# Performance work log

Hardware: AMD Instinct MI355X
Metric: run time of the kernel (lower is better)

Reference implementation:

```python
import jax, jax.numpy as jnp
import numpy as np

N, K, C_S, C_Z, C_G, H, NUM_RBF = 768, 32, 384, 128, 16, 4, 64
E = N * K
DH = C_Z // H  # 32
LN_EPS = 1e-5
DIST_EPS = 1e-8


def _rbf(D, D_min=0.0, D_max=20.0, D_count=NUM_RBF):
    # Gaussian radial basis expansion (GVP/ProteinMPNN style)
    mu = jnp.linspace(D_min, D_max, D_count, dtype=D.dtype)
    sigma = (D_max - D_min) / D_count
    return jnp.exp(-(((D[..., None] - mu) / sigma) ** 2))


def setup_inputs() -> dict:
    key = jax.random.key(0)
    ks = jax.random.split(key, 24)
    node_features = jax.random.normal(ks[0], (N, C_S), dtype=jnp.float32)
    node_trans = jax.random.uniform(ks[1], (N, 3), dtype=jnp.float32) * 30.0  # coords in a 30A box
    edge_features = jax.random.normal(ks[2], (E, C_Z), dtype=jnp.float32)
    src = jax.random.randint(ks[3], (E,), 0, N)
    dst = jnp.repeat(jnp.arange(N), K)  # sorted-by-destination layout (assume_sorted)
    edge_index = jnp.stack([src, dst]).astype(jnp.int64)

    def lin(k, fan_in, fan_out, scale=0.02):
        return jax.random.normal(k, (fan_in, fan_out), dtype=jnp.float32) * scale

    return {
        "node_features": node_features,
        "node_trans": node_trans,
        "edge_features": edge_features,
        "edge_index": edge_index,
        "w_left": lin(ks[4], C_S, C_G), "b_left": jnp.zeros((C_G,), jnp.float32),
        "w_right": lin(ks[5], C_S, C_G), "b_right": jnp.zeros((C_G,), jnp.float32),
        "w_bgate": lin(ks[6], C_G * C_G, C_Z), "b_bgate": jnp.zeros((C_Z,), jnp.float32),
        "w_dist": lin(ks[7], NUM_RBF, C_Z), "b_dist": jnp.zeros((C_Z,), jnp.float32),
        "w_tobias": lin(ks[8], C_Z, H),
        "ln_g": jnp.ones((C_Z,), jnp.float32), "ln_b": jnp.zeros((C_Z,), jnp.float32),
        "w_q": lin(ks[9], C_Z, C_Z), "b_q": jnp.zeros((C_Z,), jnp.float32),
        "w_kv": lin(ks[10], C_Z, 2 * C_Z), "b_kv": jnp.zeros((2 * C_Z,), jnp.float32),
        "w_out": lin(ks[11], C_Z, C_Z), "b_out": jnp.zeros((C_Z,), jnp.float32),
        "w_ogate": lin(ks[12], C_Z, C_Z), "b_ogate": jnp.zeros((C_Z,), jnp.float32),
    }


def reference(node_features, node_trans, edge_features, edge_index,
              w_left, b_left, w_right, b_right, w_bgate, b_bgate,
              w_dist, b_dist, w_tobias, ln_g, ln_b,
              w_q, b_q, w_kv, b_kv, w_out, b_out, w_ogate, b_ogate):
    # sparse -> knn graph (edges pre-sorted by destination, exactly K per node)
    knn_idx = edge_index[0].reshape(N, K)            # [N, K] source node of each neighbor edge
    feat = edge_features.reshape(N, K, C_Z)          # [N, K, c_z]

    # LayerNorm over c_z
    mu = feat.mean(-1, keepdims=True)
    var = feat.var(-1, keepdims=True)
    z = (feat - mu) * jax.lax.rsqrt(var + LN_EPS) * ln_g + ln_b  # [N, K, c_z]

    # outer-product gating bias
    nl = node_features @ w_left + b_left             # [N, c_gate_s]
    nr = node_features @ w_right + b_right
    e1 = nl[knn_idx]                                 # [N, K, c_gate_s]
    e2 = nr[knn_idx]
    edge3 = jnp.einsum('nik,njl->nijkl', e1, e2).reshape(N, K, K, C_G * C_G)
    gate = edge3 @ w_bgate + b_bgate                 # [N, K, K, c_z]

    # RBF distance bias
    t = node_trans[knn_idx]                          # [N, K, 3]
    diff = t[:, :, None, :] - t[:, None, :, :] + DIST_EPS
    dist = jnp.sqrt(jnp.sum(diff * diff, axis=-1))   # [N, K, K]
    db = _rbf(dist) @ w_dist + b_dist                # [N, K, K, c_z]
    bias = (jax.nn.sigmoid(gate) * db) @ w_tobias    # [N, K, K, H]

    # attention over the K neighbors of each node
    q = (z @ w_q + b_q).reshape(N, K, H, DH)
    kv = z @ w_kv + b_kv
    k_ = kv[..., :C_Z].reshape(N, K, H, DH)
    v = kv[..., C_Z:].reshape(N, K, H, DH)
    scores = jnp.einsum('nihd,njhd->nhij', q, k_) / jnp.sqrt(jnp.asarray(DH, q.dtype))
    scores = scores + bias.transpose(0, 3, 1, 2)     # [N, H, K, K] (mask all-True -> no -inf term)
    p = jax.nn.softmax(scores, axis=-1)
    o = jnp.einsum('nhij,njhd->nihd', p, v).reshape(N, K, C_Z)

    # output gate + projection, then knn -> sparse (identity reshape: full mask, sorted edges)
    o = o * jax.nn.sigmoid(z @ w_ogate + b_ogate)
    out = (o @ w_out + b_out).reshape(E, C_Z)
    return out
```

## Files before the change

kernel.cpp:

```cpp
#include <hip/hip_runtime.h>

#define NN   768
#define KKN  32
#define CS   384
#define CZ   128
#define CG   16
#define NH   4
#define DHD  32
#define NRBF 64
#define EE   (NN*KKN)

#define RBF_STEP    (20.0f/63.0f)
#define RBF_INVSTEP (63.0f/20.0f)
#define RBF_INVSIG  3.2f
#define RBF_SI      (RBF_STEP*RBF_INVSIG)

typedef __attribute__((ext_vector_type(8))) short bf16x8;
typedef __attribute__((ext_vector_type(4))) float f32x4;

__device__ __forceinline__ float bfl(unsigned int u){ return __uint_as_float(u << 16); }
__device__ __forceinline__ float bfh(unsigned int u){ return __uint_as_float(u & 0xFFFF0000u); }
__device__ __forceinline__ unsigned int packbf(float a, float b){
  unsigned int r;
  asm("v_cvt_pk_bf16_f32 %0, %1, %2" : "=v"(r) : "v"(a), "v"(b));
  return r;
}
__device__ __forceinline__ float fastrcp(float x){
  float r;
  asm("v_rcp_f32 %0, %1" : "=v"(r) : "v"(x));
  return r;
}
__device__ __forceinline__ float sigm(float x){ return fastrcp(1.0f + __expf(-x)); }

__global__ __launch_bounds__(256) void k0_prep(
    const float* __restrict__ wq, const float* __restrict__ wkv,
    const float* __restrict__ wog, const float* __restrict__ wout,
    const float* __restrict__ wd, const float* __restrict__ wt,
    const float* __restrict__ wb,
    unsigned short* __restrict__ wqkvogT, unsigned short* __restrict__ woutT,
    unsigned short* __restrict__ wdT, unsigned short* __restrict__ wtT,
    unsigned short* __restrict__ wbP, float* __restrict__ nlzero)
{
  int id = blockIdx.x*256 + threadIdx.x;
  float v[8];
  if (id < 8192){
    int c = id & 511, g = id >> 9;
    const float* src; int ld, col;
    if (c < 128){ src = wq; ld = 128; col = c; }
    else if (c < 384){ src = wkv; ld = 256; col = c-128; }
    else { src = wog; ld = 128; col = c-384; }
    #pragma unroll
    for (int j=0;j<8;j++) v[j] = src[(size_t)(g*8+j)*ld + col];
    *(uint4*)(wqkvogT + c*128 + ((g + c)&15)*8) = make_uint4(
      packbf(v[0],v[1]),packbf(v[2],v[3]),packbf(v[4],v[5]),packbf(v[6],v[7]));
  } else if (id < 10240){
    int l = id - 8192; int c = l & 127, g = l >> 7;
    #pragma unroll
    for (int j=0;j<8;j++) v[j] = wout[(size_t)(g*8+j)*128 + c];
    *(uint4*)(woutT + c*128 + ((g + c)&15)*8) = make_uint4(
      packbf(v[0],v[1]),packbf(v[2],v[3]),packbf(v[4],v[5]),packbf(v[6],v[7]));
  } else if (id < 11392){
    int l = id - 10240; int c = l & 127, g = l >> 7;
    #pragma unroll
    for (int j=0;j<8;j++) v[j] = (g<8) ? wd[(size_t)(g*8+j)*128 + c] : 0.f;
    *(uint4*)(wdT + c*72 + g*8) = make_uint4(
      packbf(v[0],v[1]),packbf(v[2],v[3]),packbf(v[4],v[5]),packbf(v[6],v[7]));
  } else if (id < 11460){
    int l = id - 11392; int h = l / 17, g = l % 17;
    #pragma unroll
    for (int j=0;j<8;j++){ int cc = g*8+j; v[j] = (cc<128)? wt[cc*4 + h] : 0.f; }
    *(uint4*)(wtT + h*136 + g*8) = make_uint4(
      packbf(v[0],v[1]),packbf(v[2],v[3]),packbf(v[4],v[5]),packbf(v[6],v[7]));
  } else if (id < 15556){
    int l2 = id - 11460;
    int c = l2 >> 5, sl = l2 & 31;
    int kl0 = sl*8;
    #pragma unroll
    for (int j=0;j<8;j++) v[j] = wb[(size_t)(kl0+j)*128 + c];
    *(uint4*)(wbP + c*256 + kl0) = make_uint4(
      packbf(v[0],v[1]),packbf(v[2],v[3]),packbf(v[4],v[5]),packbf(v[6],v[7]));
  } else if (id < 21700){
    int z = id - 15556;
    ((float4*)nlzero)[z] = make_float4(0.f,0.f,0.f,0.f);
  }
}

__global__ __launch_bounds__(256) void k1_pre(
    const float* __restrict__ nf, const float* __restrict__ ef,
    const float* __restrict__ wl, const float* __restrict__ bl,
    const float* __restrict__ wr, const float* __restrict__ br,
    const float* __restrict__ lng, const float* __restrict__ lnb,
    float* __restrict__ nlw, float* __restrict__ nrw,
    unsigned short* __restrict__ zw)
{
  int b = blockIdx.x, t = threadIdx.x;
  if (b < 1536){
    int rl = t >> 4, l16 = t & 15;
    size_t e = (size_t)b*16 + rl;
    const float4* row = (const float4*)(ef + e*CZ);
    float4 x0 = row[l16*2], x1 = row[l16*2+1];
    float v[8] = {x0.x,x0.y,x0.z,x0.w,x1.x,x1.y,x1.z,x1.w};
    float s = 0.f, q = 0.f;
    #pragma unroll
    for (int u=0;u<8;u++){ s += v[u]; q += v[u]*v[u]; }
    #pragma unroll
    for (int m=1;m<16;m<<=1){ s += __shfl_xor(s,m); q += __shfl_xor(q,m); }
    float mean = s*(1.f/128.f);
    float var  = q*(1.f/128.f) - mean*mean;
    float rs = rsqrtf(var + 1e-5f);
    int c0 = l16*8;
    unsigned int pk[4];
    #pragma unroll
    for (int u=0;u<4;u++){
      float z0 = (v[2*u]  -mean)*rs*lng[c0+2*u]   + lnb[c0+2*u];
      float z1 = (v[2*u+1]-mean)*rs*lng[c0+2*u+1] + lnb[c0+2*u+1];
      pk[u] = packbf(z0,z1);
    }
    ((uint4*)(zw + e*CZ))[l16] = make_uint4(pk[0],pk[1],pk[2],pk[3]);
  } else {
    int blk2 = b - 1536;
    int seg = blk2 / 96;
    int within = blk2 - seg*96;
    int gid = within*256 + t;
    int side = (gid >= 12288) ? 1 : 0;
    int idx = gid - side*12288;
    int nd = idx >> 4, c = idx & 15;
    const float* w = side ? wr : wl;
    float acc = (seg==0) ? (side ? br[c] : bl[c]) : 0.f;
    const float* nrow = nf + (size_t)nd*CS;
    int kb = seg*96;
    #pragma unroll 4
    for (int k=kb;k<kb+96;k++) acc += nrow[k]*w[k*CG+c];
    atomicAdd((side? nrw : nlw)+idx, acc);
  }
}

__global__ __launch_bounds__(256) void k1b_sprep(
    const float* __restrict__ nlw, const float* __restrict__ nrw,
    const unsigned short* __restrict__ wbP,
    unsigned short* __restrict__ S_all, unsigned short* __restrict__ nrb)
{
  int n = blockIdx.x, t = threadIdx.x;
  float e1[16];
  #pragma unroll
  for (int k=0;k<16;k++) e1[k] = nlw[n*CG + k];
  int c = t>>1, l0 = (t&1)*8;
  float S[8];
  #pragma unroll
  for (int u=0;u<8;u++) S[u]=0.f;
  const unsigned short* wrow = wbP + c*256 + l0;
  #pragma unroll 4
  for (int k=0;k<16;k++){
    uint4 wv = *(const uint4*)(wrow + k*16);
    float wf[8] = { bfl(wv.x), bfh(wv.x), bfl(wv.y), bfh(wv.y),
                    bfl(wv.z), bfh(wv.z), bfl(wv.w), bfh(wv.w) };
    float ev = e1[k];
    #pragma unroll
    for (int u=0;u<8;u++) S[u] += ev*wf[u];
  }
  *(uint4*)(S_all + (size_t)n*2048 + c*16 + l0) = make_uint4(
    packbf(S[0],S[1]), packbf(S[2],S[3]), packbf(S[4],S[5]), packbf(S[6],S[7]));
  if (t < 8){
    *(unsigned int*)(nrb + n*CG + 2*t) = packbf(nrw[n*CG + 2*t], nrw[n*CG + 2*t + 1]);
  }
}

__global__ __launch_bounds__(256,4) void k2_bias(
    const long long* __restrict__ eidx, const float* __restrict__ trans,
    const unsigned short* __restrict__ S_all, const unsigned short* __restrict__ nrb,
    const unsigned short* __restrict__ wdTg, const unsigned short* __restrict__ wtTg,
    const float* __restrict__ bg, const float* __restrict__ bd,
    float* __restrict__ biasw)
{
  int n = blockIdx.x >> 3, chunk = blockIdx.x & 7;
  int i0 = chunk*4;
  int t = threadIdx.x;
  int wave = t>>6, lane = t&63, q = lane>>4, l15 = lane&15;

  __shared__ __align__(16) unsigned short rbfb[32*72];
  __shared__ __align__(16) unsigned short Xb  [32*136];
  __shared__ __align__(16) float t3s[32][4];
  __shared__ __align__(16) float dsm[4][32];
  __shared__ int srcs[32];

  f32x4 zero4 = {0.f,0.f,0.f,0.f};
  uint4 uz = make_uint4(0,0,0,0);

  if (t < 32) srcs[t] = (int)eidx[(size_t)n*KKN + t];
  __syncthreads();
  if (t < 32){ int s = srcs[t];
    t3s[t][0]=trans[s*3]; t3s[t][1]=trans[s*3+1]; t3s[t][2]=trans[s*3+2]; }
  uint4 wdf[2][2];
  #pragma unroll
  for (int mt=0;mt<2;mt++){
    #pragma unroll
    for (int ks=0;ks<2;ks++)
      wdf[mt][ks] = *(const uint4*)(wdTg + (wave*32+mt*16+l15)*72 + ks*32 + q*8);
  }
  uint4 wtf[4];
  #pragma unroll
  for (int ks=0;ks<4;ks++)
    wtf[ks] = *(const uint4*)(wtTg + (l15&3)*136 + ks*32 + q*8);
  uint4 bE[2];
  #pragma unroll
  for (int nt=0;nt<2;nt++){
    int jn = srcs[nt*16 + l15];
    bE[nt] = (q < 2) ? *(const uint4*)(nrb + jn*CG + q*8) : uz;
  }
  __syncthreads();
  if (t < 128){
    int ii=t>>5, j=t&31;
    float dx=t3s[i0+ii][0]-t3s[j][0]+1e-8f;
    float dy=t3s[i0+ii][1]-t3s[j][1]+1e-8f;
    float dz=t3s[i0+ii][2]-t3s[j][2]+1e-8f;
    dsm[ii][j]=sqrtf(dx*dx+dy*dy+dz*dz);
  }
  __syncthreads();

  int jr = t>>3, sl = t&7;
  int c0base = wave*32 + q*4;

  #pragma unroll 1
  for (int ii=0; ii<4; ii++){
    int s_i = srcs[i0+ii];
    uint4 aS[2];
    #pragma unroll
    for (int mt=0;mt<2;mt++)
      aS[mt] = (q < 2) ? *(const uint4*)(S_all + (size_t)s_i*2048 + (wave*32+mt*16+l15)*16 + q*8) : uz;
    {
      float dI = dsm[ii][jr]*RBF_INVSIG;
      float e[8];
      #pragma unroll
      for (int u=0;u<8;u++){
        float x = fmaf((float)(sl*8+u), -RBF_SI, dI);
        e[u] = __expf(-x*x);
      }
      *(uint4*)&rbfb[jr*72 + sl*8] = make_uint4(
        packbf(e[0],e[1]), packbf(e[2],e[3]), packbf(e[4],e[5]), packbf(e[6],e[7]));
    }
    __syncthreads();

    f32x4 ga[2][2], da[2][2];
    #pragma unroll
    for(int a=0;a<2;a++){
      #pragma unroll
      for(int b2=0;b2<2;b2++){ ga[a][b2]=zero4; da[a][b2]=zero4; }
    }
    #pragma unroll
    for(int mt=0;mt<2;mt++){
      #pragma unroll
      for(int nt=0;nt<2;nt++)
        ga[mt][nt] = __builtin_amdgcn_mfma_f32_16x16x32_bf16(
          *(const bf16x8*)&aS[mt], *(const bf16x8*)&bE[nt], ga[mt][nt], 0,0,0);
    }
    #pragma unroll
    for(int ks=0;ks<2;ks++){
      bf16x8 bR[2];
      #pragma unroll
      for(int nt=0;nt<2;nt++) bR[nt] = *(const bf16x8*)&rbfb[(nt*16+l15)*72 + ks*32 + q*8];
      #pragma unroll
      for(int mt=0;mt<2;mt++){
        #pragma unroll
        for(int nt=0;nt<2;nt++)
          da[mt][nt] = __builtin_amdgcn_mfma_f32_16x16x32_bf16(
            *(const bf16x8*)&wdf[mt][ks], bR[nt], da[mt][nt], 0,0,0);
      }
    }
    #pragma unroll
    for(int mt=0;mt<2;mt++){
      int c0 = c0base + mt*16;
      float4 bgv = *(const float4*)(bg + c0);
      float4 bdv = *(const float4*)(bd + c0);
      #pragma unroll
      for(int nt=0;nt<2;nt++){
        float x0 = sigm(ga[mt][nt][0]+bgv.x)*(da[mt][nt][0]+bdv.x);
        float x1 = sigm(ga[mt][nt][1]+bgv.y)*(da[mt][nt][1]+bdv.y);
        float x2 = sigm(ga[mt][nt][2]+bgv.z)*(da[mt][nt][2]+bdv.z);
        float x3 = sigm(ga[mt][nt][3]+bgv.w)*(da[mt][nt][3]+bdv.w);
        *(uint2*)&Xb[(nt*16+l15)*136 + c0] = make_uint2(packbf(x0,x1), packbf(x2,x3));
      }
    }
    __syncthreads();

    if (wave < 2){
      f32x4 bacc = {0.f,0.f,0.f,0.f};
      #pragma unroll
      for(int ks=0;ks<4;ks++){
        bf16x8 bX = *(const bf16x8*)&Xb[(wave*16+l15)*136 + ks*32 + q*8];
        bacc = __builtin_amdgcn_mfma_f32_16x16x32_bf16(*(const bf16x8*)&wtf[ks], bX, bacc, 0,0,0);
      }
      if (q==0){
        int j = wave*16 + l15;
        float* base = biasw + (((size_t)n*4)*32 + (i0+ii))*32 + j;
        base[0] = bacc[0]; base[1024] = bacc[1]; base[2048] = bacc[2]; base[3072] = bacc[3];
      }
    }
  }
}

__global__ __launch_bounds__(256,3) void k3_attn(
    const unsigned short* __restrict__ zw, const float* __restrict__ biasw,
    const unsigned short* __restrict__ wqkvogT, const unsigned short* __restrict__ woutT,
    const float* __restrict__ bq, const float* __restrict__ bkv, const float* __restrict__ bog,
    const float* __restrict__ bout, float* __restrict__ out)
{
  int n = blockIdx.x, t = threadIdx.x;
  int w = t>>6, lane = t&63, q = lane>>4, l15 = lane&15;
  int i3 = lane>>1, jh = lane&1;

  __shared__ __align__(16) char smem[49152];
  uint4* wdst = (uint4*)(smem + 32768);
  unsigned short* wtS = (unsigned short*)(smem + 32768);
  f32x4 zero4 = {0.f,0.f,0.f,0.f};

  bf16x8 zfr[2][4];
  #pragma unroll
  for (int nt=0;nt<2;nt++){
    const unsigned short* zr = zw + ((size_t)n*32 + nt*16 + l15)*128;
    #pragma unroll
    for (int ks=0;ks<4;ks++) zfr[nt][ks] = *(const bf16x8*)(zr + ks*32 + q*8);
  }
  f32x4 br4[4];
  {
    const f32x4* bsrc = (const f32x4*)(biasw + (((size_t)n*4 + w)*32 + i3)*32 + jh*16);
    #pragma unroll
    for (int u=0;u<4;u++) br4[u] = bsrc[u];
  }
  const float* bseg = (w==0)? bq : (w==1)? bkv : (w==2)? (bkv+128) : bog;

  const uint4* wsrc = (const uint4*)wqkvogT;
  int sb = w*2048, db = w*256;
  uint4 sreg[4];
  #pragma unroll
  for (int u=0;u<4;u++) sreg[u] = wsrc[sb + u*64 + lane];
  const unsigned short* arow = wtS + w*2048 + l15*128;
  for (int r=0;r<8;r++){
    #pragma unroll
    for (int u=0;u<4;u++) wdst[db + u*64 + lane] = sreg[u];
    if (r<7){
      #pragma unroll
      for (int u=0;u<4;u++) sreg[u] = wsrc[sb + (r+1)*256 + u*64 + lane];
    }
    float4 bv = *(const float4*)(bseg + r*16 + q*4);
    f32x4 acc0 = zero4, acc1 = zero4;
    int cg = w*128 + r*16 + l15;
    #pragma unroll
    for (int ks=0;ks<4;ks++){
      bf16x8 af = *(const bf16x8*)(arow + (((ks*4+q) + cg)&15)*8);
      acc0 = __builtin_amdgcn_mfma_f32_16x16x32_bf16(af, zfr[0][ks], acc0, 0,0,0);
      acc1 = __builtin_amdgcn_mfma_f32_16x16x32_bf16(af, zfr[1][ks], acc1, 0,0,0);
    }
    #pragma unroll
    for (int nt=0;nt<2;nt++){
      f32x4 a = nt? acc1 : acc0;
      float v0,v1,v2,v3;
      if (w==3){ v0=sigm(a[0]+bv.x); v1=sigm(a[1]+bv.y); v2=sigm(a[2]+bv.z); v3=sigm(a[3]+bv.w); }
      else     { v0=a[0]+bv.x; v1=a[1]+bv.y; v2=a[2]+bv.z; v3=a[3]+bv.w; }
      int i = nt*16 + l15;
      int blk = ((r*2 + (q>>1)) + i) & 15;
      *(uint2*)(smem + w*8192 + i*256 + blk*16 + (q&1)*8) = make_uint2(packbf(v0,v1), packbf(v2,v3));
    }
  }
  __syncthreads();

  float sc[16];
  {
    float qreg[32];
    #pragma unroll
    for (int dq=0;dq<4;dq++){
      uint4 qa = *(const uint4*)(smem + i3*256 + (((w*4+dq) + i3)&15)*16);
      unsigned int qu[4] = {qa.x,qa.y,qa.z,qa.w};
      #pragma unroll
      for (int u2=0;u2<4;u2++){ qreg[dq*8+2*u2]=bfl(qu[u2]); qreg[dq*8+2*u2+1]=bfh(qu[u2]); }
    }
    int j0 = jh*16;
    #pragma unroll
    for (int jj=0;jj<16;jj++){
      int j = j0+jj;
      float s = 0.f;
      #pragma unroll
      for (int dq=0;dq<4;dq++){
        uint4 ka = *(const uint4*)(smem + 8192 + j*256 + (((w*4+dq) + j)&15)*16);
        unsigned int ku[4] = {ka.x,ka.y,ka.z,ka.w};
        #pragma unroll
        for (int u2=0;u2<4;u2++)
          s += qreg[dq*8+2*u2]*bfl(ku[u2]) + qreg[dq*8+2*u2+1]*bfh(ku[u2]);
      }
      sc[jj] = s*0.17677669529663687f + br4[jj>>2][jj&3];
    }
  }
  {
    float mx = sc[0];
    #pragma unroll
    for (int jj=1;jj<16;jj++) mx = fmaxf(mx, sc[jj]);
    mx = fmaxf(mx, __shfl_xor(mx,1));
    float sum = 0.f;
    #pragma unroll
    for (int jj=0;jj<16;jj++){ sc[jj] = __expf(sc[jj]-mx); sum += sc[jj]; }
    sum += __shfl_xor(sum,1);
    float inv = fastrcp(sum);
    #pragma unroll
    for (int jj=0;jj<16;jj++) sc[jj] *= inv;
  }
  __syncthreads();
  {
    int dbase = w*32 + jh*16;
    int db8 = dbase >> 3;
    float o16[16];
    #pragma unroll
    for (int u=0;u<16;u++) o16[u]=0.f;
    #pragma unroll
    for (int j=0;j<32;j++){
      float pj = __shfl(sc[j & 15], (lane & 62) | (j >> 4));
      uint4 va0 = *(const uint4*)(smem + 16384 + j*256 + (((db8+0) + j)&15)*16);
      uint4 va1 = *(const uint4*)(smem + 16384 + j*256 + (((db8+1) + j)&15)*16);
      unsigned int vu[8] = {va0.x,va0.y,va0.z,va0.w,va1.x,va1.y,va1.z,va1.w};
      #pragma unroll
      for (int u2=0;u2<8;u2++){ o16[2*u2] += pj*bfl(vu[u2]); o16[2*u2+1] += pj*bfh(vu[u2]); }
    }
    uint4 ga0 = *(const uint4*)(smem + 24576 + i3*256 + (((db8+0) + i3)&15)*16);
    uint4 ga1 = *(const uint4*)(smem + 24576 + i3*256 + (((db8+1) + i3)&15)*16);
    unsigned int gu[8] = {ga0.x,ga0.y,ga0.z,ga0.w,ga1.x,ga1.y,ga1.z,ga1.w};
    #pragma unroll
    for (int u2=0;u2<8;u2++){
      float y0 = o16[2*u2]  *bfl(gu[u2]);
      float y1 = o16[2*u2+1]*bfh(gu[u2]);
      int c = dbase + 2*u2;
      *(unsigned int*)(smem + i3*256 + (((c>>3) + i3)&15)*16 + (c&7)*2) = packbf(y0,y1);
    }
  }
  __syncthreads();

  bf16x8 yfr[2][4];
  #pragma unroll
  for (int mt=0;mt<2;mt++){
    int row = mt*16 + l15;
    #pragma unroll
    for (int ks=0;ks<4;ks++)
      yfr[mt][ks] = *(const bf16x8*)(smem + row*256 + (((ks*4+q) + row)&15)*16);
  }
  const uint4* osrc = (const uint4*)woutT;
  #pragma unroll
  for (int r2=0;r2<2;r2++){
    int c0 = (r2*4 + w)*16;
    #pragma unroll
    for (int u=0;u<4;u++) wdst[db + u*64 + lane] = osrc[c0*16 + u*64 + lane];
    int cg2 = c0 + l15;
    const unsigned short* brow = wtS + w*2048 + l15*128;
    f32x4 oa0 = zero4, oa1 = zero4;
    #pragma unroll
    for (int ks=0;ks<4;ks++){
      bf16x8 bf = *(const bf16x8*)(brow + (((ks*4+q) + cg2)&15)*8);
      oa0 = __builtin_amdgcn_mfma_f32_16x16x32_bf16(yfr[0][ks], bf, oa0, 0,0,0);
      oa1 = __builtin_amdgcn_mfma_f32_16x16x32_bf16(yfr[1][ks], bf, oa1, 0,0,0);
    }
    float bov = bout[cg2];
    #pragma unroll
    for (int mt=0;mt<2;mt++){
      f32x4 oa = mt? oa1 : oa0;
      #pragma unroll
      for (int rg=0; rg<4; rg++){
        int i = mt*16 + q*4 + rg;
        out[((size_t)n*32 + i)*128 + cg2] = oa[rg] + bov;
      }
    }
  }
}

extern "C" void kernel_launch(void* const* d_in, const int* in_sizes, int n_in,
                              void* d_out, int out_size, void* d_ws, size_t ws_size,
                              hipStream_t stream)
{
  const float* nf  = (const float*)d_in[0];
  const float* tr  = (const float*)d_in[1];
  const float* ef  = (const float*)d_in[2];
  const long long* ei = (const long long*)d_in[3];
  const float* wl  = (const float*)d_in[4];  const float* bl  = (const float*)d_in[5];
  const float* wr  = (const float*)d_in[6];  const float* br  = (const float*)d_in[7];
  const float* wbg = (const float*)d_in[8];  const float* bbg = (const float*)d_in[9];
  const float* wdi = (const float*)d_in[10]; const float* bdi = (const float*)d_in[11];
  const float* wtb = (const float*)d_in[12];
  const float* lng = (const float*)d_in[13]; const float* lnb = (const float*)d_in[14];
  const float* wq  = (const float*)d_in[15]; const float* bq  = (const float*)d_in[16];
  const float* wkv = (const float*)d_in[17]; const float* bkv = (const float*)d_in[18];
  const float* wo  = (const float*)d_in[19]; const float* bo  = (const float*)d_in[20];
  const float* wog = (const float*)d_in[21]; const float* bog = (const float*)d_in[22];
  float* outp = (float*)d_out;
  float* ws = (float*)d_ws;
  float* nlw = ws;
  float* nrw = ws + 12288;
  float* biasw = ws + 24576;
  unsigned short* zw      = (unsigned short*)(ws + 3170304);
  unsigned short* wqkvogT = (unsigned short*)(ws + 4743168);
  unsigned short* woutT   = (unsigned short*)(ws + 4775936);
  unsigned short* wdTg    = (unsigned short*)(ws + 4784128);
  unsigned short* wtTg    = (unsigned short*)(ws + 4788736);
  unsigned short* wbPg    = (unsigned short*)(ws + 4789824);
  unsigned short* S_all   = (unsigned short*)(ws + 4806208);
  unsigned short* nrb     = (unsigned short*)(ws + 5592640);

  hipLaunchKernelGGL(k0_prep, dim3(85), dim3(256), 0, stream,
                     wq, wkv, wog, wo, wdi, wtb, wbg, wqkvogT, woutT, wdTg, wtTg, wbPg, nlw);
  hipLaunchKernelGGL(k1_pre, dim3(1920), dim3(256), 0, stream,
                     nf, ef, wl, bl, wr, br, lng, lnb, nlw, nrw, zw);
  hipLaunchKernelGGL(k1b_sprep, dim3(768), dim3(256), 0, stream,
                     nlw, nrw, wbPg, S_all, nrb);
  hipLaunchKernelGGL(k2_bias, dim3(6144), dim3(256), 0, stream,
                     ei, tr, S_all, nrb, wdTg, wtTg, bbg, bdi, biasw);
  hipLaunchKernelGGL(k3_attn, dim3(768), dim3(256), 0, stream,
                     zw, biasw, wqkvogT, woutT, bq, bkv, bog, bo, outp);
}
```

Before: 224.7 us.

## Double-buffer bias kernel, fuse node projections into sprep, drop atomics

The bias kernel now handles 8 query rows per block instead of 4, halving its grid. It double-buffers the RBF and X tiles in XOR-swizzled unpadded LDS and prefetches the next row's S operands, so the final wtobias MFMA of one row overlaps the next row and one barrier per iteration is removed. The left/right node projections move from the atomic-based k1_pre path into k1b_sprep using a shuffle reduction, which removes the zeroing pass and the atomics. The sigmoid is rewritten with exp2 and a folded bias, at the cost of more LDS and registers per block.

```diff
diff --git a/kernel.cpp b/kernel.cpp
--- a/kernel.cpp
+++ b/kernel.cpp
@@ -14,6 +14,7 @@
 #define RBF_INVSTEP (63.0f/20.0f)
 #define RBF_INVSIG  3.2f
 #define RBF_SI      (RBF_STEP*RBF_INVSIG)
+#define L2E         1.44269504f
 
 typedef __attribute__((ext_vector_type(8))) short bf16x8;
 typedef __attribute__((ext_vector_type(4))) float f32x4;
@@ -39,7 +40,7 @@
     const float* __restrict__ wb,
     unsigned short* __restrict__ wqkvogT, unsigned short* __restrict__ woutT,
     unsigned short* __restrict__ wdT, unsigned short* __restrict__ wtT,
-    unsigned short* __restrict__ wbP, float* __restrict__ nlzero)
+    unsigned short* __restrict__ wbP)
 {
   int id = blockIdx.x*256 + threadIdx.x;
   float v[8];
@@ -79,71 +80,67 @@
     for (int j=0;j<8;j++) v[j] = wb[(size_t)(kl0+j)*128 + c];
     *(uint4*)(wbP + c*256 + kl0) = make_uint4(
       packbf(v[0],v[1]),packbf(v[2],v[3]),packbf(v[4],v[5]),packbf(v[6],v[7]));
-  } else if (id < 21700){
-    int z = id - 15556;
-    ((float4*)nlzero)[z] = make_float4(0.f,0.f,0.f,0.f);
   }
 }
 
 __global__ __launch_bounds__(256) void k1_pre(
-    const float* __restrict__ nf, const float* __restrict__ ef,
-    const float* __restrict__ wl, const float* __restrict__ bl,
-    const float* __restrict__ wr, const float* __restrict__ br,
+    const float* __restrict__ ef,
     const float* __restrict__ lng, const float* __restrict__ lnb,
-    float* __restrict__ nlw, float* __restrict__ nrw,
     unsigned short* __restrict__ zw)
 {
   int b = blockIdx.x, t = threadIdx.x;
-  if (b < 1536){
-    int rl = t >> 4, l16 = t & 15;
-    size_t e = (size_t)b*16 + rl;
-    const float4* row = (const float4*)(ef + e*CZ);
-    float4 x0 = row[l16*2], x1 = row[l16*2+1];
-    float v[8] = {x0.x,x0.y,x0.z,x0.w,x1.x,x1.y,x1.z,x1.w};
-    float s = 0.f, q = 0.f;
-    #pragma unroll
-    for (int u=0;u<8;u++){ s += v[u]; q += v[u]*v[u]; }
-    #pragma unroll
-    for (int m=1;m<16;m<<=1){ s += __shfl_xor(s,m); q += __shfl_xor(q,m); }
-    float mean = s*(1.f/128.f);
-    float var  = q*(1.f/128.f) - mean*mean;
-    float rs = rsqrtf(var + 1e-5f);
-    int c0 = l16*8;
-    unsigned int pk[4];
-    #pragma unroll
-    for (int u=0;u<4;u++){
-      float z0 = (v[2*u]  -mean)*rs*lng[c0+2*u]   + lnb[c0+2*u];
-      float z1 = (v[2*u+1]-mean)*rs*lng[c0+2*u+1] + lnb[c0+2*u+1];
-      pk[u] = packbf(z0,z1);
-    }
-    ((uint4*)(zw + e*CZ))[l16] = make_uint4(pk[0],pk[1],pk[2],pk[3]);
-  } else {
-    int blk2 = b - 1536;
-    int seg = blk2 / 96;
-    int within = blk2 - seg*96;
-    int gid = within*256 + t;
-    int side = (gid >= 12288) ? 1 : 0;
-    int idx = gid - side*12288;
-    int nd = idx >> 4, c = idx & 15;
-    const float* w = side ? wr : wl;
-    float acc = (seg==0) ? (side ? br[c] : bl[c]) : 0.f;
-    const float* nrow = nf + (size_t)nd*CS;
-    int kb = seg*96;
-    #pragma unroll 4
-    for (int k=kb;k<kb+96;k++) acc += nrow[k]*w[k*CG+c];
-    atomicAdd((side? nrw : nlw)+idx, acc);
-  }
+  int rl = t >> 4, l16 = t & 15;
+  size_t e = (size_t)b*16 + rl;
+  const float4* row = (const float4*)(ef + e*CZ);
+  float4 x0 = row[l16*2], x1 = row[l16*2+1];
+  float v[8] = {x0.x,x0.y,x0.z,x0.w,x1.x,x1.y,x1.z,x1.w};
+  float s = 0.f, q = 0.f;
+  #pragma unroll
+  for (int u=0;u<8;u++){ s += v[u]; q += v[u]*v[u]; }
+  #pragma unroll
+  for (int m=1;m<16;m<<=1){ s += __shfl_xor(s,m); q += __shfl_xor(q,m); }
+  float mean = s*(1.f/128.f);
+  float var  = q*(1.f/128.f) - mean*mean;
+  float rs = rsqrtf(var + 1e-5f);
+  int c0 = l16*8;
+  unsigned int pk[4];
+  #pragma unroll
+  for (int u=0;u<4;u++){
+    float z0 = (v[2*u]  -mean)*rs*lng[c0+2*u]   + lnb[c0+2*u];
+    float z1 = (v[2*u+1]-mean)*rs*lng[c0+2*u+1] + lnb[c0+2*u+1];
+    pk[u] = packbf(z0,z1);
+  }
+  ((uint4*)(zw + e*CZ))[l16] = make_uint4(pk[0],pk[1],pk[2],pk[3]);
 }
 
 __global__ __launch_bounds__(256) void k1b_sprep(
-    const float* __restrict__ nlw, const float* __restrict__ nrw,
+    const float* __restrict__ nf,
+    const float* __restrict__ wl, const float* __restrict__ bl,
+    const float* __restrict__ wr, const float* __restrict__ br,
     const unsigned short* __restrict__ wbP,
     unsigned short* __restrict__ S_all, unsigned short* __restrict__ nrb)
 {
   int n = blockIdx.x, t = threadIdx.x;
+  __shared__ float nlS[16], nrS[16];
+  {
+    int c = t >> 4, sl = t & 15;
+    const float* nrow = nf + (size_t)n*CS + sl*24;
+    float aL = 0.f, aR = 0.f;
+    #pragma unroll 4
+    for (int u=0; u<24; u++){
+      float x = nrow[u];
+      int k = sl*24 + u;
+      aL = fmaf(x, wl[k*CG + c], aL);
+      aR = fmaf(x, wr[k*CG + c], aR);
+    }
+    #pragma unroll
+    for (int m=1;m<16;m<<=1){ aL += __shfl_xor(aL,m); aR += __shfl_xor(aR,m); }
+    if (sl == 0){ nlS[c] = aL + bl[c]; nrS[c] = aR + br[c]; }
+  }
+  __syncthreads();
   float e1[16];
   #pragma unroll
-  for (int k=0;k<16;k++) e1[k] = nlw[n*CG + k];
+  for (int k=0;k<16;k++) e1[k] = nlS[k];
   int c = t>>1, l0 = (t&1)*8;
   float S[8];
   #pragma unroll
@@ -156,12 +153,12 @@
                     bfl(wv.z), bfh(wv.z), bfl(wv.w), bfh(wv.w) };
     float ev = e1[k];
     #pragma unroll
-    for (int u=0;u<8;u++) S[u] += ev*wf[u];
+    for (int u=0;u<8;u++) S[u] = fmaf(ev, wf[u], S[u]);
   }
   *(uint4*)(S_all + (size_t)n*2048 + c*16 + l0) = make_uint4(
     packbf(S[0],S[1]), packbf(S[2],S[3]), packbf(S[4],S[5]), packbf(S[6],S[7]));
   if (t < 8){
-    *(unsigned int*)(nrb + n*CG + 2*t) = packbf(nrw[n*CG + 2*t], nrw[n*CG + 2*t + 1]);
+    *(unsigned int*)(nrb + n*CG + 2*t) = packbf(nrS[2*t], nrS[2*t+1]);
   }
 }
 
@@ -172,15 +169,15 @@
     const float* __restrict__ bg, const float* __restrict__ bd,
     float* __restrict__ biasw)
 {
-  int n = blockIdx.x >> 3, chunk = blockIdx.x & 7;
-  int i0 = chunk*4;
+  int n = blockIdx.x >> 2, chunk = blockIdx.x & 3;
+  int i0 = chunk*8;
   int t = threadIdx.x;
   int wave = t>>6, lane = t&63, q = lane>>4, l15 = lane&15;
 
-  __shared__ __align__(16) unsigned short rbfb[32*72];
-  __shared__ __align__(16) unsigned short Xb  [32*136];
+  __shared__ __align__(16) unsigned short rbfb[2][32*64];
+  __shared__ __align__(16) unsigned short Xb  [2][32*128];
   __shared__ __align__(16) float t3s[32][4];
-  __shared__ __align__(16) float dsm[4][32];
+  __shared__ __align__(16) float dsm[8][32];
   __shared__ int srcs[32];
 
   f32x4 zero4 = {0.f,0.f,0.f,0.f};
@@ -208,25 +205,45 @@
     bE[nt] = (q < 2) ? *(const uint4*)(nrb + jn*CG + q*8) : uz;
   }
   __syncthreads();
-  if (t < 128){
-    int ii=t>>5, j=t&31;
-    float dx=t3s[i0+ii][0]-t3s[j][0]+1e-8f;
-    float dy=t3s[i0+ii][1]-t3s[j][1]+1e-8f;
-    float dz=t3s[i0+ii][2]-t3s[j][2]+1e-8f;
-    dsm[ii][j]=sqrtf(dx*dx+dy*dy+dz*dz);
+  {
+    int di = t>>5, j = t&31;
+    float dx=t3s[i0+di][0]-t3s[j][0]+1e-8f;
+    float dy=t3s[i0+di][1]-t3s[j][1]+1e-8f;
+    float dz=t3s[i0+di][2]-t3s[j][2]+1e-8f;
+    dsm[di][j]=sqrtf(dx*dx+dy*dy+dz*dz);
   }
   __syncthreads();
 
   int jr = t>>3, sl = t&7;
   int c0base = wave*32 + q*4;
-
-  #pragma unroll 1
-  for (int ii=0; ii<4; ii++){
-    int s_i = srcs[i0+ii];
-    uint4 aS[2];
+  int swz  = l15 & 7;
+  int wswz = jr & 7;
+
+  auto do_final = [&](int fi, int pb){
+    f32x4 bacc = {0.f,0.f,0.f,0.f};
+    #pragma unroll
+    for (int ks=0;ks<4;ks++){
+      bf16x8 bX = *(const bf16x8*)&Xb[pb][(wave*16+l15)*128 + ((((ks<<2)+q) ^ swz)<<3)];
+      bacc = __builtin_amdgcn_mfma_f32_16x16x32_bf16(*(const bf16x8*)&wtf[ks], bX, bacc, 0,0,0);
+    }
+    if (q==0){
+      int j = wave*16 + l15;
+      float* base = biasw + (((size_t)n*4)*32 + (i0+fi))*32 + j;
+      base[0] = bacc[0]; base[1024] = bacc[1]; base[2048] = bacc[2]; base[3072] = bacc[3];
+    }
+  };
+
+  uint4 aS[2], aSn[2];
+  {
+    int s_i = srcs[i0];
     #pragma unroll
     for (int mt=0;mt<2;mt++)
       aS[mt] = (q < 2) ? *(const uint4*)(S_all + (size_t)s_i*2048 + (wave*32+mt*16+l15)*16 + q*8) : uz;
+  }
+
+  #pragma unroll 1
+  for (int ii=0; ii<8; ii++){
+    int p = ii & 1;
     {
       float dI = dsm[ii][jr]*RBF_INVSIG;
       float e[8];
@@ -235,8 +252,14 @@
         float x = fmaf((float)(sl*8+u), -RBF_SI, dI);
         e[u] = __expf(-x*x);
       }
-      *(uint4*)&rbfb[jr*72 + sl*8] = make_uint4(
+      *(uint4*)&rbfb[p][jr*64 + ((sl ^ wswz)<<3)] = make_uint4(
         packbf(e[0],e[1]), packbf(e[2],e[3]), packbf(e[4],e[5]), packbf(e[6],e[7]));
+    }
+    if (ii < 7){
+      int s_n = srcs[i0+ii+1];
+      #pragma unroll
+      for (int mt=0;mt<2;mt++)
+        aSn[mt] = (q < 2) ? *(const uint4*)(S_all + (size_t)s_n*2048 + (wave*32+mt*16+l15)*16 + q*8) : uz;
     }
     __syncthreads();
 
@@ -257,7 +280,8 @@
     for(int ks=0;ks<2;ks++){
       bf16x8 bR[2];
       #pragma unroll
-      for(int nt=0;nt<2;nt++) bR[nt] = *(const bf16x8*)&rbfb[(nt*16+l15)*72 + ks*32 + q*8];
+      for(int nt=0;nt<2;nt++)
+        bR[nt] = *(const bf16x8*)&rbfb[p][(nt*16+l15)*64 + ((((ks<<2)+q) ^ swz)<<3)];
       #pragma unroll
       for(int mt=0;mt<2;mt++){
         #pragma unroll
@@ -266,36 +290,30 @@
             *(const bf16x8*)&wdf[mt][ks], bR[nt], da[mt][nt], 0,0,0);
       }
     }
-    #pragma unroll
-    for(int mt=0;mt<2;mt++){
-      int c0 = c0base + mt*16;
-      float4 bgv = *(const float4*)(bg + c0);
-      float4 bdv = *(const float4*)(bd + c0);
-      #pragma unroll
-      for(int nt=0;nt<2;nt++){
-        float x0 = sigm(ga[mt][nt][0]+bgv.x)*(da[mt][nt][0]+bdv.x);
-        float x1 = sigm(ga[mt][nt][1]+bgv.y)*(da[mt][nt][1]+bdv.y);
-        float x2 = sigm(ga[mt][nt][2]+bgv.z)*(da[mt][nt][2]+bdv.z);
-        float x3 = sigm(ga[mt][nt][3]+bgv.w)*(da[mt][nt][3]+bdv.w);
-        *(uint2*)&Xb[(nt*16+l15)*136 + c0] = make_uint2(packbf(x0,x1), packbf(x2,x3));
+    {
+      unsigned short* Xc = Xb[p];
+      #pragma unroll
+      for(int mt=0;mt<2;mt++){
+        int c0 = c0base + mt*16;
+        float4 bgv = *(const float4*)(bg + c0);
+        float4 bdv = *(const float4*)(bd + c0);
+        float4 bgn; bgn.x = bgv.x*-L2E; bgn.y = bgv.y*-L2E; bgn.z = bgv.z*-L2E; bgn.w = bgv.w*-L2E;
+        int ch = ((c0>>3) ^ swz);
+        #pragma unroll
+        for(int nt=0;nt<2;nt++){
+          float x0 = fastrcp(1.f + exp2f(fmaf(ga[mt][nt][0], -L2E, bgn.x)))*(da[mt][nt][0]+bdv.x);
+          float x1 = fastrcp(1.f + exp2f(fmaf(ga[mt][nt][1], -L2E, bgn.y)))*(da[mt][nt][1]+bdv.y);
+          float x2 = fastrcp(1.f + exp2f(fmaf(ga[mt][nt][2], -L2E, bgn.z)))*(da[mt][nt][2]+bdv.z);
+          float x3 = fastrcp(1.f + exp2f(fmaf(ga[mt][nt][3], -L2E, bgn.w)))*(da[mt][nt][3]+bdv.w);
+          *(uint2*)&Xc[(nt*16+l15)*128 + (ch<<3) + (q&1)*4] = make_uint2(packbf(x0,x1), packbf(x2,x3));
+        }
       }
     }
-    __syncthreads();
-
-    if (wave < 2){
-      f32x4 bacc = {0.f,0.f,0.f,0.f};
-      #pragma unroll
-      for(int ks=0;ks<4;ks++){
-        bf16x8 bX = *(const bf16x8*)&Xb[(wave*16+l15)*136 + ks*32 + q*8];
-        bacc = __builtin_amdgcn_mfma_f32_16x16x32_bf16(*(const bf16x8*)&wtf[ks], bX, bacc, 0,0,0);
-      }
-      if (q==0){
-        int j = wave*16 + l15;
-        float* base = biasw + (((size_t)n*4)*32 + (i0+ii))*32 + j;
-        base[0] = bacc[0]; base[1024] = bacc[1]; base[2048] = bacc[2]; base[3072] = bacc[3];
-      }
-    }
-  }
+    if (ii > 0 && wave < 2) do_final(ii-1, p^1);
+    aS[0] = aSn[0]; aS[1] = aSn[1];
+  }
+  __syncthreads();
+  if (wave < 2) do_final(7, 1);
 }
 
 __global__ __launch_bounds__(256,3) void k3_attn(
@@ -487,8 +505,6 @@
   const float* wog = (const float*)d_in[21]; const float* bog = (const float*)d_in[22];
   float* outp = (float*)d_out;
   float* ws = (float*)d_ws;
-  float* nlw = ws;
-  float* nrw = ws + 12288;
   float* biasw = ws + 24576;
   unsigned short* zw      = (unsigned short*)(ws + 3170304);
   unsigned short* wqkvogT = (unsigned short*)(ws + 4743168);
@@ -499,13 +515,13 @@
   unsigned short* S_all   = (unsigned short*)(ws + 4806208);
   unsigned short* nrb     = (unsigned short*)(ws + 5592640);
 
-  hipLaunchKernelGGL(k0_prep, dim3(85), dim3(256), 0, stream,
-                     wq, wkv, wog, wo, wdi, wtb, wbg, wqkvogT, woutT, wdTg, wtTg, wbPg, nlw);
-  hipLaunchKernelGGL(k1_pre, dim3(1920), dim3(256), 0, stream,
-                     nf, ef, wl, bl, wr, br, lng, lnb, nlw, nrw, zw);
+  hipLaunchKernelGGL(k0_prep, dim3(61), dim3(256), 0, stream,
+                     wq, wkv, wog, wo, wdi, wtb, wbg, wqkvogT, woutT, wdTg, wtTg, wbPg);
+  hipLaunchKernelGGL(k1_pre, dim3(1536), dim3(256), 0, stream,
+                     ef, lng, lnb, zw);
   hipLaunchKernelGGL(k1b_sprep, dim3(768), dim3(256), 0, stream,
-                     nlw, nrw, wbPg, S_all, nrb);
-  hipLaunchKernelGGL(k2_bias, dim3(6144), dim3(256), 0, stream,
+                     nf, wl, bl, wr, br, wbPg, S_all, nrb);
+  hipLaunchKernelGGL(k2_bias, dim3(3072), dim3(256), 0, stream,
                      ei, tr, S_all, nrb, wdTg, wtTg, bbg, bdi, biasw);
   hipLaunchKernelGGL(k3_attn, dim3(768), dim3(256), 0, stream,
                      zw, biasw, wqkvogT, woutT, bq, bkv, bog, bo, outp);
```

New measurement: 239.9 us. 1.07x slower.
